# Performance work log

Measured on AMD Instinct MI355X. Metric: run time of the kernel, lower is better.

The kernel has to match this reference:

```python
import jax, jax.numpy as jnp
import numpy as np
from jax import lax

DN = ('NCHW', 'OIHW', 'NCHW')


def _conv(x, w, pad):
    return lax.conv_general_dilated(x, w, (1, 1), [(pad, pad), (pad, pad)], dimension_numbers=DN)


def _bn(x, gamma, beta, mean, var, eps=1e-5):
    inv = gamma * lax.rsqrt(var + eps)
    return x * inv[None, :, None, None] + (beta - mean * inv)[None, :, None, None]


def _unfold(x, K, pad):
    # torch.nn.Unfold layout: channel-major, kernel positions fastest -> (B, C, K*K, H, W)
    B, C, H, W = x.shape
    p = lax.conv_general_dilated_patches(x, (K, K), (1, 1), [(pad, pad), (pad, pad)], dimension_numbers=DN)
    return p.reshape(B, C, K * K, H, W)


def setup_inputs() -> dict:
    key = jax.random.key(0)
    ks = jax.random.split(key, 16)
    B, C, H, W, K = 16, 64, 64, 64, 3
    d = {
        'x': jax.random.normal(ks[0], (B, C, H, W), jnp.float32),
        'wq': jax.random.normal(ks[1], (C, C, 1, 1), jnp.float32) * 0.1,
        'wk': jax.random.normal(ks[2], (C, C, K, K), jnp.float32) * 0.05,
        'wv': jax.random.normal(ks[3], (C, C, 1, 1), jnp.float32) * 0.1,
        'pos_h': jax.random.normal(ks[4], (C, K, 1), jnp.float32),
        'pos_w': jax.random.normal(ks[5], (C, 1, K), jnp.float32),
    }
    for i, nm in enumerate(['q', 'k', 'v', 'o']):
        d[nm + '_gamma'] = jnp.ones((C,), jnp.float32)
        d[nm + '_beta'] = jnp.zeros((C,), jnp.float32)
        d[nm + '_mean'] = jax.random.normal(ks[6 + i], (C,), jnp.float32) * 0.1
        d[nm + '_var'] = jax.random.uniform(ks[10 + i], (C,), jnp.float32, 0.5, 1.5)
    return d


def reference(x, wq, q_gamma, q_beta, q_mean, q_var,
              wk, k_gamma, k_beta, k_mean, k_var,
              wv, v_gamma, v_beta, v_mean, v_var,
              pos_h, pos_w, o_gamma, o_beta, o_mean, o_var):
    B, C, H, W = x.shape
    K = pos_h.shape[1]
    heads = C // 8
    cph = C // heads  # channels per head

    q = jax.nn.relu(_bn(_conv(x, wq, 0), q_gamma, q_beta, q_mean, q_var))
    k = jax.nn.relu(_bn(_conv(x, wk, K // 2), k_gamma, k_beta, k_mean, k_var))
    v = _bn(_conv(x, wv, 0), v_gamma, v_beta, v_mean, v_var)

    # local keys + positional bias: (B, C, K*K, H, W)
    unfold_k = _unfold(k, K, K // 2)
    pos = (pos_h + pos_w).reshape(1, C, K * K, 1, 1)
    kp = (unfold_k + pos).reshape(B, heads, cph, K * K, H, W)
    qh = q.reshape(B, heads, cph, 1, H, W)

    attn = (qh * kp).sum(axis=2)            # (B, heads, K*K, H, W)
    attn = jax.nn.softmax(attn, axis=2)

    # local aggregation (LocalConvolution): weights shared across cph channels per head
    uv = _unfold(v, K, (K - 1) // 2).reshape(B, heads, cph, K * K, H, W)
    out = (attn[:, :, None] * uv).sum(axis=3).reshape(B, C, H, W)

    out = jax.nn.relu(_bn(out, o_gamma, o_beta, o_mean, o_var))
    return out
```

## Files before the change

### kernel.cpp

```cpp
#include <hip/hip_runtime.h>
#include <hip/hip_bf16.h>
#include <math.h>

#define B_ 16
#define C_ 64
#define H_ 64
#define W_ 64
#define KSTEPS 18

typedef __attribute__((ext_vector_type(8))) short bf16x8;
typedef __attribute__((ext_vector_type(4))) float f32x4;

static __device__ __forceinline__ unsigned short f2b(float f) {
    __hip_bfloat16 h = __float2bfloat16(f);
    return *reinterpret_cast<unsigned short*>(&h);
}
static __device__ __forceinline__ float b2f(unsigned short u) {
    __hip_bfloat16 h;
    *reinterpret_cast<unsigned short*>(&h) = u;
    return __bfloat162float(h);
}

__global__ __launch_bounds__(64) void prep_kernel(
    const float* __restrict__ wq, const float* __restrict__ wk, const float* __restrict__ wv,
    const float* __restrict__ qg, const float* __restrict__ qb, const float* __restrict__ qm, const float* __restrict__ qv,
    const float* __restrict__ kg, const float* __restrict__ kb, const float* __restrict__ km, const float* __restrict__ kv,
    const float* __restrict__ vg, const float* __restrict__ vb, const float* __restrict__ vm, const float* __restrict__ vv,
    const float* __restrict__ og, const float* __restrict__ ob, const float* __restrict__ om, const float* __restrict__ ov,
    unsigned short* __restrict__ Wp, float* __restrict__ bnp)
{
    const int bid = blockIdx.x;
    const int lane = threadIdx.x;
    if (bid < 12 * KSTEPS) {
        const int mf = bid / KSTEPS;
        const int ks = bid % KSTEPS;
        const int r = lane & 15;
        bf16x8 u;
#pragma unroll
        for (int j = 0; j < 8; j++) {
            int k = ks * 32 + ((lane >> 4) << 3) + j;
            int tap = k >> 6;
            int c = k & 63;
            float w;
            if (mf < 4)      { int co = mf * 16 + r;        w = (tap == 4) ? wq[co * 64 + c] : 0.f; }
            else if (mf < 8) { int co = (mf - 4) * 16 + r;  w = wk[(co * 64 + c) * 9 + tap]; }
            else             { int co = (mf - 8) * 16 + r;  w = (tap == 4) ? wv[co * 64 + c] : 0.f; }
            u[j] = (short)f2b(w);
        }
        *reinterpret_cast<bf16x8*>(Wp + ((size_t)(mf * KSTEPS + ks) * 64 + lane) * 8) = u;
    } else {
        const int c = lane;
        const float* G[4] = {qg, kg, vg, og};
        const float* Bt[4] = {qb, kb, vb, ob};
        const float* M[4] = {qm, km, vm, om};
        const float* V[4] = {qv, kv, vv, ov};
#pragma unroll
        for (int p = 0; p < 4; p++) {
            float inv = G[p][c] * rsqrtf(V[p][c] + 1e-5f);
            bnp[p * 128 + c] = inv;
            bnp[p * 128 + 64 + c] = Bt[p][c] - M[p][c] * inv;
        }
    }
}

__global__ __launch_bounds__(256) void qkv_mfma(
    const float* __restrict__ x, const unsigned short* __restrict__ Wp,
    const float* __restrict__ bnp,
    unsigned short* __restrict__ qt, unsigned short* __restrict__ kt, unsigned short* __restrict__ vt)
{
    __shared__ __align__(16) char smem[64 * 196 * 4];
    const int bid = blockIdx.x;
    const int b = bid >> 6;
    const int h = bid & 63;
    const int tid = threadIdx.x;

    for (int i = tid; i < 3 * 66 * 8; i += 256) {
        int col = i % 66;
        int dy  = (i / 66) % 3;
        int c0g = i / 198;
        int gh = h + dy - 1, gw = col - 1;
        bool ok = ((unsigned)gh < 64u) && ((unsigned)gw < 64u);
        bf16x8 u;
#pragma unroll
        for (int j = 0; j < 8; j++) {
            float f = ok ? x[((b * 64 + c0g * 8 + j) * 64 + gh) * 64 + gw] : 0.f;
            u[j] = (short)f2b(f);
        }
        int La = ((dy * 66 + col) * 64 + c0g * 8) * 2;
        La ^= (col & 7) << 4;
        *reinterpret_cast<bf16x8*>(smem + La) = u;
    }
    __syncthreads();

    const int wid = tid >> 6, lane = tid & 63;
    f32x4 acc[3][4];
#pragma unroll
    for (int m = 0; m < 3; m++)
#pragma unroll
        for (int nf = 0; nf < 4; nf++) acc[m][nf] = (f32x4){0.f, 0.f, 0.f, 0.f};

    for (int ks = 0; ks < KSTEPS; ks++) {
        const int tap = ks >> 1;
        const int dy = tap / 3, dx = tap - dy * 3;
        const int c0 = (ks & 1) * 32 + ((lane >> 4) << 3);
        bf16x8 bf[4];
#pragma unroll
        for (int nf = 0; nf < 4; nf++) {
            int col = nf * 16 + (lane & 15) + dx;
            int La = ((dy * 66 + col) * 64 + c0) * 2;
            La ^= (col & 7) << 4;
            bf[nf] = *reinterpret_cast<const bf16x8*>(smem + La);
        }
#pragma unroll
        for (int m = 0; m < 3; m++) {
            int mf = wid * 3 + m;
            bf16x8 af = *reinterpret_cast<const bf16x8*>(Wp + ((size_t)(mf * KSTEPS + ks) * 64 + lane) * 8);
#pragma unroll
            for (int nf = 0; nf < 4; nf++)
                acc[m][nf] = __builtin_amdgcn_mfma_f32_16x16x32_bf16(af, bf[nf], acc[m][nf], 0, 0, 0);
        }
    }
    __syncthreads();

    float* xp = reinterpret_cast<float*>(smem);
#pragma unroll
    for (int m = 0; m < 3; m++) {
        int mf = wid * 3 + m;
        int plane = mf >> 2;
#pragma unroll
        for (int nf = 0; nf < 4; nf++) {
            int px = nf * 16 + (lane & 15);
            int cobase = mf * 16 + ((lane >> 4) << 2);
#pragma unroll
            for (int r = 0; r < 3 + 1; r++) {
                int c = (cobase + r) & 63;
                float inv = bnp[plane * 128 + c];
                float bias = bnp[plane * 128 + 64 + c];
                float val = acc[m][nf][r] * inv + bias;
                if (plane < 2) val = fmaxf(val, 0.f);
                xp[px * 196 + cobase + r] = val;
            }
        }
    }
    __syncthreads();

    if (tid < 192) {
        int px = tid & 63, plane = tid >> 6;
        unsigned short* dst = (plane == 0 ? qt : plane == 1 ? kt : vt)
                              + ((size_t)((b * 64 + h) * 64 + px)) * 64;
        for (int j = 0; j < 64; j += 8) {
            bf16x8 u;
#pragma unroll
            for (int t = 0; t < 8; t++)
                u[t] = (short)f2b(xp[px * 196 + plane * 64 + j + t]);
            *reinterpret_cast<bf16x8*>(dst + j) = u;
        }
    }
}

__global__ __launch_bounds__(256) void attn2_kernel(
    const unsigned short* __restrict__ qt, const unsigned short* __restrict__ kt,
    const unsigned short* __restrict__ vt,
    const float* __restrict__ ph, const float* __restrict__ pw,
    const float* __restrict__ bnp, float* __restrict__ out)
{
    const int bid = blockIdx.x;
    const int hh = bid & 1;
    const int h = (bid >> 1) & 63;
    const int b = bid >> 7;
    const int px = threadIdx.x & 63;
    const int head = hh * 4 + (threadIdx.x >> 6);
    const int cb = head * 8;

    float qf[8];
    {
        bf16x8 q8 = *reinterpret_cast<const bf16x8*>(qt + ((size_t)((b * 64 + h) * 64 + px)) * 64 + cb);
#pragma unroll
        for (int j = 0; j < 8; j++) qf[j] = b2f((unsigned short)q8[j]);
    }

    float A[3], Bx[3];
#pragma unroll
    for (int t = 0; t < 3; t++) {
        float a = 0.f, bb = 0.f;
#pragma unroll
        for (int j = 0; j < 8; j++) {
            a  = fmaf(qf[j], ph[(cb + j) * 3 + t], a);
            bb = fmaf(qf[j], pw[(cb + j) * 3 + t], bb);
        }
        A[t] = a; Bx[t] = bb;
    }

    float logit[9];
#pragma unroll
    for (int ky = 0; ky < 3; ky++) {
        int gh = h + ky - 1;
        bool rok = (unsigned)gh < 64u;
#pragma unroll
        for (int kx = 0; kx < 3; kx++) {
            int gw = px + kx - 1;
            bool ok = rok && ((unsigned)gw < 64u);
            float qk = 0.f;
            if (ok) {
                bf16x8 k8 = *reinterpret_cast<const bf16x8*>(kt + ((size_t)((b * 64 + gh) * 64 + gw)) * 64 + cb);
#pragma unroll
                for (int j = 0; j < 8; j++) qk = fmaf(qf[j], b2f((unsigned short)k8[j]), qk);
            }
            logit[ky * 3 + kx] = qk + A[ky] + Bx[kx];
        }
    }

    float m = logit[0];
#pragma unroll
    for (int t = 1; t < 9; t++) m = fmaxf(m, logit[t]);
    float e[9], sum = 0.f;
#pragma unroll
    for (int t = 0; t < 9; t++) { e[t] = __expf(logit[t] - m); sum += e[t]; }
    float inv = 1.f / sum;

    float o[8];
#pragma unroll
    for (int j = 0; j < 8; j++) o[j] = 0.f;
#pragma unroll
    for (int ky = 0; ky < 3; ky++) {
        int gh = h + ky - 1;
        bool rok = (unsigned)gh < 64u;
#pragma unroll
        for (int kx = 0; kx < 3; kx++) {
            int gw = px + kx - 1;
            if (rok && ((unsigned)gw < 64u)) {
                bf16x8 v8 = *reinterpret_cast<const bf16x8*>(vt + ((size_t)((b * 64 + gh) * 64 + gw)) * 64 + cb);
                float w = e[ky * 3 + kx];
#pragma unroll
                for (int j = 0; j < 8; j++) o[j] = fmaf(w, b2f((unsigned short)v8[j]), o[j]);
            }
        }
    }

#pragma unroll
    for (int j = 0; j < 8; j++) {
        int c = cb + j;
        float io = bnp[3 * 128 + c];
        float bo = bnp[3 * 128 + 64 + c];
        float val = fmaxf(fmaf(o[j] * inv, io, bo), 0.f);
        out[((size_t)(b * C_ + c) * H_ + h) * W_ + px] = val;
    }
}

extern "C" void kernel_launch(void* const* d_in, const int* in_sizes, int n_in,
                              void* d_out, int out_size, void* d_ws, size_t ws_size,
                              hipStream_t stream)
{
    const float* x   = (const float*)d_in[0];
    const float* wq  = (const float*)d_in[1];
    const float* wk  = (const float*)d_in[2];
    const float* wv  = (const float*)d_in[3];
    const float* ph  = (const float*)d_in[4];
    const float* pw  = (const float*)d_in[5];
    const float* qg  = (const float*)d_in[6];
    const float* qb  = (const float*)d_in[7];
    const float* qm  = (const float*)d_in[8];
    const float* qv  = (const float*)d_in[9];
    const float* kg  = (const float*)d_in[10];
    const float* kb  = (const float*)d_in[11];
    const float* km  = (const float*)d_in[12];
    const float* kv  = (const float*)d_in[13];
    const float* vg  = (const float*)d_in[14];
    const float* vb  = (const float*)d_in[15];
    const float* vm  = (const float*)d_in[16];
    const float* vv  = (const float*)d_in[17];
    const float* og  = (const float*)d_in[18];
    const float* ob  = (const float*)d_in[19];
    const float* om  = (const float*)d_in[20];
    const float* ov  = (const float*)d_in[21];

    char* ws = (char*)d_ws;
    unsigned short* Wp = (unsigned short*)ws;
    float* bnp = (float*)(ws + 221184);
    unsigned short* qt = (unsigned short*)(ws + 223232);
    unsigned short* kt = qt + (size_t)B_ * H_ * W_ * C_;
    unsigned short* vt = kt + (size_t)B_ * H_ * W_ * C_;

    prep_kernel<<<12 * KSTEPS + 1, 64, 0, stream>>>(
        wq, wk, wv, qg, qb, qm, qv, kg, kb, km, kv, vg, vb, vm, vv,
        og, ob, om, ov, Wp, bnp);

    qkv_mfma<<<B_ * H_, 256, 0, stream>>>(x, Wp, bnp, qt, kt, vt);

    attn2_kernel<<<B_ * H_ * 2, 256, 0, stream>>>(qt, kt, vt, ph, pw, bnp, (float*)d_out);
}
```

Before: 188.6 us.

## Process two rows per QKV block, store directly, and stage K/V halos in LDS

The QKV MFMA kernel now handles two output rows per 512-thread block. This shares a 4-row input halo instead of loading 3 rows for each single row, and it removes the LDS transpose epilogue by writing packed bf16x4 results straight to global memory. The attention kernel now stages the 3-row K and V neighbourhoods with zero padding into swizzled LDS once per row for all 8 heads, which removes bounds checks and repeated global gathers. The costs are larger LDS per block, which may lower occupancy, and less-coalesced 8-byte global stores in the QKV epilogue.

```diff
diff --git a/kernel.cpp b/kernel.cpp
--- a/kernel.cpp
+++ b/kernel.cpp
@@ -9,6 +9,7 @@
 #define KSTEPS 18
 
 typedef __attribute__((ext_vector_type(8))) short bf16x8;
+typedef __attribute__((ext_vector_type(4))) short bf16x4;
 typedef __attribute__((ext_vector_type(4))) float f32x4;
 
 static __device__ __forceinline__ unsigned short f2b(float f) {
@@ -63,22 +64,23 @@
     }
 }
 
-__global__ __launch_bounds__(256) void qkv_mfma(
+__global__ __launch_bounds__(512) void qkv_mfma2(
     const float* __restrict__ x, const unsigned short* __restrict__ Wp,
     const float* __restrict__ bnp,
     unsigned short* __restrict__ qt, unsigned short* __restrict__ kt, unsigned short* __restrict__ vt)
 {
-    __shared__ __align__(16) char smem[64 * 196 * 4];
+    __shared__ __align__(16) char xs[4 * 66 * 64 * 2];
+    __shared__ float bns[384];
     const int bid = blockIdx.x;
-    const int b = bid >> 6;
-    const int h = bid & 63;
+    const int b  = bid >> 5;
+    const int h0 = (bid & 31) << 1;
     const int tid = threadIdx.x;
 
-    for (int i = tid; i < 3 * 66 * 8; i += 256) {
+    for (int i = tid; i < 4 * 66 * 8; i += 512) {
         int col = i % 66;
-        int dy  = (i / 66) % 3;
-        int c0g = i / 198;
-        int gh = h + dy - 1, gw = col - 1;
+        int dy  = (i / 66) & 3;
+        int c0g = i / 264;
+        int gh = h0 - 1 + dy, gw = col - 1;
         bool ok = ((unsigned)gh < 64u) && ((unsigned)gw < 64u);
         bf16x8 u;
 #pragma unroll
@@ -88,88 +90,106 @@
         }
         int La = ((dy * 66 + col) * 64 + c0g * 8) * 2;
         La ^= (col & 7) << 4;
-        *reinterpret_cast<bf16x8*>(smem + La) = u;
-    }
+        *reinterpret_cast<bf16x8*>(xs + La) = u;
+    }
+    if (tid < 384) bns[tid] = bnp[tid];
     __syncthreads();
 
     const int wid = tid >> 6, lane = tid & 63;
+    const int mfg = wid >> 1, nfg = wid & 1;
+    const int t = lane & 15, q4 = lane >> 4;
+
     f32x4 acc[3][4];
 #pragma unroll
     for (int m = 0; m < 3; m++)
 #pragma unroll
-        for (int nf = 0; nf < 4; nf++) acc[m][nf] = (f32x4){0.f, 0.f, 0.f, 0.f};
+        for (int n = 0; n < 4; n++) acc[m][n] = (f32x4){0.f, 0.f, 0.f, 0.f};
 
     for (int ks = 0; ks < KSTEPS; ks++) {
         const int tap = ks >> 1;
         const int dy = tap / 3, dx = tap - dy * 3;
-        const int c0 = (ks & 1) * 32 + ((lane >> 4) << 3);
+        const int kb = (ks & 1) * 32 + q4 * 8;
         bf16x8 bf[4];
 #pragma unroll
-        for (int nf = 0; nf < 4; nf++) {
-            int col = nf * 16 + (lane & 15) + dx;
-            int La = ((dy * 66 + col) * 64 + c0) * 2;
+        for (int n = 0; n < 4; n++) {
+            int p = (nfg * 4 + n) * 16 + t;
+            int r = p >> 6, colw = p & 63;
+            int col = colw + dx;
+            int La = (((r + dy) * 66 + col) * 64 + kb) * 2;
             La ^= (col & 7) << 4;
-            bf[nf] = *reinterpret_cast<const bf16x8*>(smem + La);
+            bf[n] = *reinterpret_cast<const bf16x8*>(xs + La);
         }
 #pragma unroll
         for (int m = 0; m < 3; m++) {
-            int mf = wid * 3 + m;
+            int mf = mfg * 3 + m;
             bf16x8 af = *reinterpret_cast<const bf16x8*>(Wp + ((size_t)(mf * KSTEPS + ks) * 64 + lane) * 8);
 #pragma unroll
-            for (int nf = 0; nf < 4; nf++)
-                acc[m][nf] = __builtin_amdgcn_mfma_f32_16x16x32_bf16(af, bf[nf], acc[m][nf], 0, 0, 0);
-        }
-    }
-    __syncthreads();
-
-    float* xp = reinterpret_cast<float*>(smem);
+            for (int n = 0; n < 4; n++)
+                acc[m][n] = __builtin_amdgcn_mfma_f32_16x16x32_bf16(af, bf[n], acc[m][n], 0, 0, 0);
+        }
+    }
+
 #pragma unroll
     for (int m = 0; m < 3; m++) {
-        int mf = wid * 3 + m;
+        int mf = mfg * 3 + m;
         int plane = mf >> 2;
-#pragma unroll
-        for (int nf = 0; nf < 4; nf++) {
-            int px = nf * 16 + (lane & 15);
-            int cobase = mf * 16 + ((lane >> 4) << 2);
-#pragma unroll
-            for (int r = 0; r < 3 + 1; r++) {
-                int c = (cobase + r) & 63;
-                float inv = bnp[plane * 128 + c];
-                float bias = bnp[plane * 128 + 64 + c];
-                float val = acc[m][nf][r] * inv + bias;
+        int co0 = mf * 16 + q4 * 4;
+        int c0 = co0 & 63;
+        f32x4 inv  = *reinterpret_cast<const f32x4*>(&bns[plane * 128 + c0]);
+        f32x4 bias = *reinterpret_cast<const f32x4*>(&bns[plane * 128 + 64 + c0]);
+        unsigned short* base = (plane == 0 ? qt : plane == 1 ? kt : vt);
+#pragma unroll
+        for (int n = 0; n < 4; n++) {
+            int p = (nfg * 4 + n) * 16 + t;
+            int r = p >> 6, colw = p & 63;
+            bf16x4 pack;
+#pragma unroll
+            for (int j = 0; j < 4; j++) {
+                float val = acc[m][n][j] * inv[j] + bias[j];
                 if (plane < 2) val = fmaxf(val, 0.f);
-                xp[px * 196 + cobase + r] = val;
+                pack[j] = (short)f2b(val);
             }
-        }
-    }
-    __syncthreads();
-
-    if (tid < 192) {
-        int px = tid & 63, plane = tid >> 6;
-        unsigned short* dst = (plane == 0 ? qt : plane == 1 ? kt : vt)
-                              + ((size_t)((b * 64 + h) * 64 + px)) * 64;
-        for (int j = 0; j < 64; j += 8) {
-            bf16x8 u;
-#pragma unroll
-            for (int t = 0; t < 8; t++)
-                u[t] = (short)f2b(xp[px * 196 + plane * 64 + j + t]);
-            *reinterpret_cast<bf16x8*>(dst + j) = u;
-        }
-    }
-}
-
-__global__ __launch_bounds__(256) void attn2_kernel(
+            *reinterpret_cast<bf16x4*>(base + ((size_t)((b * 64 + h0 + r) * 64 + colw)) * 64 + c0) = pack;
+        }
+    }
+}
+
+__global__ __launch_bounds__(512) void attn3_kernel(
     const unsigned short* __restrict__ qt, const unsigned short* __restrict__ kt,
     const unsigned short* __restrict__ vt,
     const float* __restrict__ ph, const float* __restrict__ pw,
     const float* __restrict__ bnp, float* __restrict__ out)
 {
+    __shared__ __align__(16) char ksm[3 * 66 * 64 * 2];
+    __shared__ __align__(16) char vsm[3 * 66 * 64 * 2];
+    __shared__ float bno[128];
     const int bid = blockIdx.x;
-    const int hh = bid & 1;
-    const int h = (bid >> 1) & 63;
-    const int b = bid >> 7;
-    const int px = threadIdx.x & 63;
-    const int head = hh * 4 + (threadIdx.x >> 6);
+    const int b = bid >> 6;
+    const int h = bid & 63;
+    const int tid = threadIdx.x;
+
+    for (int i = tid; i < 3 * 66 * 8; i += 512) {
+        int c8  = i & 7;
+        int pxp = (i >> 3) % 66;
+        int dy  = (i >> 3) / 66;
+        int gh = h + dy - 1, gw = pxp - 1;
+        bool ok = ((unsigned)gh < 64u) && ((unsigned)gw < 64u);
+        int La = ((dy * 66 + pxp) * 64 + c8 * 8) * 2;
+        La ^= (pxp & 7) << 4;
+        bf16x8 kk = (bf16x8){0,0,0,0,0,0,0,0}, vv = kk;
+        if (ok) {
+            size_t src = ((size_t)((b * 64 + gh) * 64 + gw)) * 64 + c8 * 8;
+            kk = *reinterpret_cast<const bf16x8*>(kt + src);
+            vv = *reinterpret_cast<const bf16x8*>(vt + src);
+        }
+        *reinterpret_cast<bf16x8*>(ksm + La) = kk;
+        *reinterpret_cast<bf16x8*>(vsm + La) = vv;
+    }
+    if (tid < 128) bno[tid] = bnp[384 + tid];
+    __syncthreads();
+
+    const int px = tid & 63;
+    const int head = tid >> 6;
     const int cb = head * 8;
 
     float qf[8];
@@ -181,68 +201,61 @@
 
     float A[3], Bx[3];
 #pragma unroll
-    for (int t = 0; t < 3; t++) {
+    for (int tt = 0; tt < 3; tt++) {
         float a = 0.f, bb = 0.f;
 #pragma unroll
         for (int j = 0; j < 8; j++) {
-            a  = fmaf(qf[j], ph[(cb + j) * 3 + t], a);
-            bb = fmaf(qf[j], pw[(cb + j) * 3 + t], bb);
-        }
-        A[t] = a; Bx[t] = bb;
+            a  = fmaf(qf[j], ph[(cb + j) * 3 + tt], a);
+            bb = fmaf(qf[j], pw[(cb + j) * 3 + tt], bb);
+        }
+        A[tt] = a; Bx[tt] = bb;
     }
 
     float logit[9];
 #pragma unroll
-    for (int ky = 0; ky < 3; ky++) {
-        int gh = h + ky - 1;
-        bool rok = (unsigned)gh < 64u;
-#pragma unroll
-        for (int kx = 0; kx < 3; kx++) {
-            int gw = px + kx - 1;
-            bool ok = rok && ((unsigned)gw < 64u);
+    for (int dy = 0; dy < 3; dy++) {
+#pragma unroll
+        for (int dx = 0; dx < 3; dx++) {
+            int pxp = px + dx;
+            int La = ((dy * 66 + pxp) * 64 + cb) * 2;
+            La ^= (pxp & 7) << 4;
+            bf16x8 k8 = *reinterpret_cast<const bf16x8*>(ksm + La);
             float qk = 0.f;
-            if (ok) {
-                bf16x8 k8 = *reinterpret_cast<const bf16x8*>(kt + ((size_t)((b * 64 + gh) * 64 + gw)) * 64 + cb);
-#pragma unroll
-                for (int j = 0; j < 8; j++) qk = fmaf(qf[j], b2f((unsigned short)k8[j]), qk);
-            }
-            logit[ky * 3 + kx] = qk + A[ky] + Bx[kx];
+#pragma unroll
+            for (int j = 0; j < 8; j++) qk = fmaf(qf[j], b2f((unsigned short)k8[j]), qk);
+            logit[dy * 3 + dx] = qk + A[dy] + Bx[dx];
         }
     }
 
     float m = logit[0];
 #pragma unroll
-    for (int t = 1; t < 9; t++) m = fmaxf(m, logit[t]);
+    for (int tt = 1; tt < 9; tt++) m = fmaxf(m, logit[tt]);
     float e[9], sum = 0.f;
 #pragma unroll
-    for (int t = 0; t < 9; t++) { e[t] = __expf(logit[t] - m); sum += e[t]; }
+    for (int tt = 0; tt < 9; tt++) { e[tt] = __expf(logit[tt] - m); sum += e[tt]; }
     float inv = 1.f / sum;
 
     float o[8];
 #pragma unroll
     for (int j = 0; j < 8; j++) o[j] = 0.f;
 #pragma unroll
-    for (int ky = 0; ky < 3; ky++) {
-        int gh = h + ky - 1;
-        bool rok = (unsigned)gh < 64u;
-#pragma unroll
-        for (int kx = 0; kx < 3; kx++) {
-            int gw = px + kx - 1;
-            if (rok && ((unsigned)gw < 64u)) {
-                bf16x8 v8 = *reinterpret_cast<const bf16x8*>(vt + ((size_t)((b * 64 + gh) * 64 + gw)) * 64 + cb);
-                float w = e[ky * 3 + kx];
-#pragma unroll
-                for (int j = 0; j < 8; j++) o[j] = fmaf(w, b2f((unsigned short)v8[j]), o[j]);
-            }
+    for (int dy = 0; dy < 3; dy++) {
+#pragma unroll
+        for (int dx = 0; dx < 3; dx++) {
+            int pxp = px + dx;
+            int La = ((dy * 66 + pxp) * 64 + cb) * 2;
+            La ^= (pxp & 7) << 4;
+            bf16x8 v8 = *reinterpret_cast<const bf16x8*>(vsm + La);
+            float w = e[dy * 3 + dx];
+#pragma unroll
+            for (int j = 0; j < 8; j++) o[j] = fmaf(w, b2f((unsigned short)v8[j]), o[j]);
         }
     }
 
 #pragma unroll
     for (int j = 0; j < 8; j++) {
         int c = cb + j;
-        float io = bnp[3 * 128 + c];
-        float bo = bnp[3 * 128 + 64 + c];
-        float val = fmaxf(fmaf(o[j] * inv, io, bo), 0.f);
+        float val = fmaxf(fmaf(o[j] * inv, bno[c], bno[64 + c]), 0.f);
         out[((size_t)(b * C_ + c) * H_ + h) * W_ + px] = val;
     }
 }
@@ -285,7 +298,7 @@
         wq, wk, wv, qg, qb, qm, qv, kg, kb, km, kv, vg, vb, vm, vv,
         og, ob, om, ov, Wp, bnp);
 
-    qkv_mfma<<<B_ * H_, 256, 0, stream>>>(x, Wp, bnp, qt, kt, vt);
-
-    attn2_kernel<<<B_ * H_ * 2, 256, 0, stream>>>(qt, kt, vt, ph, pw, bnp, (float*)d_out);
-}
+    qkv_mfma2<<<B_ * H_ / 2, 512, 0, stream>>>(x, Wp, bnp, qt, kt, vt);
+
+    attn3_kernel<<<B_ * H_, 512, 0, stream>>>(qt, kt, vt, ph, pw, bnp, (float*)d_out);
+}
```

After: 156.3 us. 17.1% less time.
